# Performance work log

Hardware: AMD Instinct MI355X
Metric: run time of the kernel (lower is better)

## Reference

```python
import jax, jax.numpy as jnp
import numpy as np

N_BOOK = 16  # == len_code; C() loop is only consistent when len_code == n_book


def setup_inputs() -> dict:
    key = jax.random.key(0)
    k1, k2 = jax.random.split(key)
    N = 32768
    D = 256        # len_code * n_book = 16 * 16
    n_classes = 4096
    features = jax.random.normal(k1, (N, D), dtype=jnp.float32)
    # Prototypes passed transposed relative to storage: [len_code*n_book, n_classes]
    Prototypes = jax.random.normal(k2, (D, n_classes), dtype=jnp.float32)
    return {"features": features, "Prototypes": Prototypes}


def reference(features, Prototypes):
    # Faithful to GPQSoftMaxNet.C: per-book matmul, concat over books, mean.
    # features: [N, len_code*n_book] split along dim 1 into chunks of width n_book
    # Prototypes: [len_code*n_book, n_classes] split along dim 0 into chunks of height n_book
    n_book = N_BOOK
    N, D = features.shape
    n_classes = Prototypes.shape[1]
    f = features.reshape(N, -1, n_book)          # [N, n_book(=len_code), n_book]
    P = Prototypes.reshape(-1, n_book, n_classes)  # [n_book(=len_code), n_book, n_classes]
    # mean over books of per-book GEMMs, fused into one einsum (no [N,C,n_book] intermediate)
    logits = jnp.einsum('nbd,bdc->nc', f, P) / jnp.float32(n_book)
    return logits
```

## Files before the change

### kernel.cpp

```cpp
#include <hip/hip_runtime.h>
#include <hip/hip_bf16.h>

typedef __attribute__((ext_vector_type(8))) short short8;
typedef __attribute__((ext_vector_type(4))) float f32x4;

static constexpr int MT = 32768;
static constexpr int KT = 256;
static constexpr int CT = 4096;

__device__ __forceinline__ unsigned short f2b(float f) {
  unsigned int b = __float_as_uint(f);
  b += 0x7FFFu + ((b >> 16) & 1u);
  return (unsigned short)(b >> 16);
}

__global__ void __launch_bounds__(256) cvt_kernel(const float* __restrict__ A,
                                                  const float* __restrict__ B,
                                                  unsigned short* __restrict__ Abf,
                                                  unsigned short* __restrict__ Bt) {
  __shared__ unsigned short tile[32][33];
  int bid = blockIdx.x, tid = threadIdx.x;
  if (bid < 4096) {
    int i = bid * 256 + tid;
    const float4 v0 = reinterpret_cast<const float4*>(A)[2 * i];
    const float4 v1 = reinterpret_cast<const float4*>(A)[2 * i + 1];
    short8 o;
    o[0] = (short)f2b(v0.x); o[1] = (short)f2b(v0.y);
    o[2] = (short)f2b(v0.z); o[3] = (short)f2b(v0.w);
    o[4] = (short)f2b(v1.x); o[5] = (short)f2b(v1.y);
    o[6] = (short)f2b(v1.z); o[7] = (short)f2b(v1.w);
    reinterpret_cast<short8*>(Abf)[i] = o;
  } else {
    int b = bid - 4096;
    int c0 = (b & 127) * 32, k0 = (b >> 7) * 32;
    int tx = tid & 31, ty0 = tid >> 5;
#pragma unroll
    for (int i = 0; i < 4; ++i) {
      int ty = ty0 + i * 8;
      tile[ty][tx] = f2b(B[(size_t)(k0 + ty) * CT + c0 + tx]);
    }
    __syncthreads();
#pragma unroll
    for (int i = 0; i < 4; ++i) {
      int cy = ty0 + i * 8;
      Bt[(size_t)(c0 + cy) * KT + k0 + tx] = tile[tx][cy];
    }
  }
}

__device__ __forceinline__ void gload16(const void* g, void* l) {
  __builtin_amdgcn_global_load_lds(
      (const __attribute__((address_space(1))) void*)g,
      (__attribute__((address_space(3))) void*)l, 16, 0, 0);
}

__global__ void __launch_bounds__(256, 2) gemm_kernel(const unsigned short* __restrict__ Abf,
                                                      const unsigned short* __restrict__ Btw,
                                                      float* __restrict__ O) {
  constexpr int BK = 64;
  __shared__ __align__(16) char smem[48 * 1024];
  unsigned short* Al = (unsigned short*)smem;
  unsigned short* Bl = (unsigned short*)(smem + 16384);
  float* eb = (float*)smem;

  int bid = blockIdx.x;
  int wg = (bid & 7) * 512 + (bid >> 3);
  int tc = wg & 15;
  int tr = wg >> 4;
  int r0 = tr * 128, c0 = tc * 256;

  int tid = threadIdx.x;
  int lane = tid & 63, wid = tid >> 6;
  int wr = wid >> 1, wc = wid & 1;
  int l15 = lane & 15, l4 = lane >> 4;

  f32x4 acc[8][4] = {};

  for (int t = 0; t < KT / BK; ++t) {
    if (t) __syncthreads();
#pragma unroll
    for (int i = 0; i < 4; ++i) {
      int c = i * 256 + wid * 64 + lane;
      int sc = (c & 7) ^ ((c >> 3) & 7);
      gload16(Abf + (size_t)(r0 + (c >> 3)) * KT + t * BK + sc * 8,
              Al + (i * 256 + wid * 64) * 8);
    }
#pragma unroll
    for (int i = 0; i < 8; ++i) {
      int c = i * 256 + wid * 64 + lane;
      int sc = (c & 7) ^ ((c >> 3) & 7);
      gload16(Btw + (size_t)(c0 + (c >> 3)) * KT + t * BK + sc * 8,
              Bl + (i * 256 + wid * 64) * 8);
    }
    __syncthreads();

#pragma unroll
    for (int ks = 0; ks < 2; ++ks) {
      short8 af[4], bf[8];
#pragma unroll
      for (int m = 0; m < 4; ++m) {
        int row = wr * 64 + m * 16 + l15;
        int slot = (ks * 4 + l4) ^ (l15 & 7);
        af[m] = *reinterpret_cast<const short8*>(Al + row * BK + slot * 8);
      }
#pragma unroll
      for (int n = 0; n < 8; ++n) {
        int row = wc * 128 + n * 16 + l15;
        int slot = (ks * 4 + l4) ^ (l15 & 7);
        bf[n] = *reinterpret_cast<const short8*>(Bl + row * BK + slot * 8);
      }
#pragma unroll
      for (int n = 0; n < 8; ++n)
#pragma unroll
        for (int m = 0; m < 4; ++m)
          acc[n][m] = __builtin_amdgcn_mfma_f32_16x16x32_bf16(bf[n], af[m], acc[n][m], 0, 0, 0);
    }
  }

  const float s = 1.0f / 16.0f;
#pragma unroll
  for (int p = 0; p < 4; ++p) {
    __syncthreads();
    if (wr == (p >> 1)) {
#pragma unroll
      for (int mm = 0; mm < 2; ++mm) {
        int m = (p & 1) * 2 + mm;
#pragma unroll
        for (int n = 0; n < 8; ++n) {
          f32x4 v = acc[n][m];
          v[0] *= s; v[1] *= s; v[2] *= s; v[3] *= s;
          *reinterpret_cast<f32x4*>(
              &eb[(mm * 16 + l15) * 264 + wc * 128 + n * 16 + l4 * 4]) = v;
        }
      }
    }
    __syncthreads();
#pragma unroll
    for (int i = 0; i < 8; ++i) {
      int r = i * 4 + wid;
      f32x4 v = *reinterpret_cast<const f32x4*>(&eb[r * 264 + lane * 4]);
      __builtin_nontemporal_store(v, reinterpret_cast<f32x4*>(
          O + (size_t)(r0 + p * 32 + r) * CT + c0 + lane * 4));
    }
  }
}

__global__ void __launch_bounds__(256) naive_kernel(const float* __restrict__ A,
                                                    const float* __restrict__ B,
                                                    float* __restrict__ O) {
  size_t i = (size_t)blockIdx.x * 256 + threadIdx.x;
  int col = (int)(i & (size_t)(CT - 1));
  int row = (int)(i >> 12);
  float s = 0.f;
  for (int k = 0; k < KT; ++k)
    s += A[(size_t)row * KT + k] * B[(size_t)k * CT + col];
  O[i] = s * (1.0f / 16.0f);
}

extern "C" void kernel_launch(void* const* d_in, const int* in_sizes, int n_in,
                              void* d_out, int out_size, void* d_ws, size_t ws_size,
                              hipStream_t stream) {
  const float* A = (const float*)d_in[0];
  const float* B = (const float*)d_in[1];
  float* O = (float*)d_out;
  const size_t needA = (size_t)MT * KT * sizeof(unsigned short);
  const size_t needB = (size_t)CT * KT * sizeof(unsigned short);
  if (ws_size >= needA + needB) {
    unsigned short* Abf = (unsigned short*)d_ws;
    unsigned short* Btw = (unsigned short*)((char*)d_ws + needA);
    cvt_kernel<<<4096 + 1024, 256, 0, stream>>>(A, B, Abf, Btw);
    gemm_kernel<<<(MT / 128) * (CT / 256), 256, 0, stream>>>(Abf, Btw, O);
  } else {
    naive_kernel<<<(unsigned)((size_t)MT * CT / 256), 256, 0, stream>>>(A, B, O);
  }
}
```

Before: 125.9 us.

## Fuse A fp32-to-bf16 conversion into GEMM tile loads

Removes the separate pass that converts features to bf16 in a workspace. The GEMM now loads fp32 A tiles straight into LDS, using a 16-slot XOR swizzle, and rounds them to bf16 in registers before each MFMA. This saves a full read and write of the converted A buffer. In exchange, A traffic into LDS doubles, each A tile is converted redundantly by all 16 column-tile workgroups, and LDS grows to 64KB, which may limit occupancy to 2 blocks.

```diff
diff --git a/kernel.cpp b/kernel.cpp
--- a/kernel.cpp
+++ b/kernel.cpp
@@ -14,37 +14,22 @@
   return (unsigned short)(b >> 16);
 }
 
-__global__ void __launch_bounds__(256) cvt_kernel(const float* __restrict__ A,
-                                                  const float* __restrict__ B,
-                                                  unsigned short* __restrict__ Abf,
-                                                  unsigned short* __restrict__ Bt) {
+__global__ void __launch_bounds__(256) cvtB_kernel(const float* __restrict__ B,
+                                                   unsigned short* __restrict__ Bt) {
   __shared__ unsigned short tile[32][33];
-  int bid = blockIdx.x, tid = threadIdx.x;
-  if (bid < 4096) {
-    int i = bid * 256 + tid;
-    const float4 v0 = reinterpret_cast<const float4*>(A)[2 * i];
-    const float4 v1 = reinterpret_cast<const float4*>(A)[2 * i + 1];
-    short8 o;
-    o[0] = (short)f2b(v0.x); o[1] = (short)f2b(v0.y);
-    o[2] = (short)f2b(v0.z); o[3] = (short)f2b(v0.w);
-    o[4] = (short)f2b(v1.x); o[5] = (short)f2b(v1.y);
-    o[6] = (short)f2b(v1.z); o[7] = (short)f2b(v1.w);
-    reinterpret_cast<short8*>(Abf)[i] = o;
-  } else {
-    int b = bid - 4096;
-    int c0 = (b & 127) * 32, k0 = (b >> 7) * 32;
-    int tx = tid & 31, ty0 = tid >> 5;
+  int b = blockIdx.x, tid = threadIdx.x;
+  int c0 = (b & 127) * 32, k0 = (b >> 7) * 32;
+  int tx = tid & 31, ty0 = tid >> 5;
 #pragma unroll
-    for (int i = 0; i < 4; ++i) {
-      int ty = ty0 + i * 8;
-      tile[ty][tx] = f2b(B[(size_t)(k0 + ty) * CT + c0 + tx]);
-    }
-    __syncthreads();
+  for (int i = 0; i < 4; ++i) {
+    int ty = ty0 + i * 8;
+    tile[ty][tx] = f2b(B[(size_t)(k0 + ty) * CT + c0 + tx]);
+  }
+  __syncthreads();
 #pragma unroll
-    for (int i = 0; i < 4; ++i) {
-      int cy = ty0 + i * 8;
-      Bt[(size_t)(c0 + cy) * KT + k0 + tx] = tile[tx][cy];
-    }
+  for (int i = 0; i < 4; ++i) {
+    int cy = ty0 + i * 8;
+    Bt[(size_t)(c0 + cy) * KT + k0 + tx] = tile[tx][cy];
   }
 }
 
@@ -54,13 +39,13 @@
       (__attribute__((address_space(3))) void*)l, 16, 0, 0);
 }
 
-__global__ void __launch_bounds__(256, 2) gemm_kernel(const unsigned short* __restrict__ Abf,
+__global__ void __launch_bounds__(256, 2) gemm_kernel(const float* __restrict__ A,
                                                       const unsigned short* __restrict__ Btw,
                                                       float* __restrict__ O) {
   constexpr int BK = 64;
-  __shared__ __align__(16) char smem[48 * 1024];
-  unsigned short* Al = (unsigned short*)smem;
-  unsigned short* Bl = (unsigned short*)(smem + 16384);
+  __shared__ __align__(16) char smem[64 * 1024];
+  float* Alf = (float*)smem;
+  unsigned short* Bl = (unsigned short*)(smem + 32768);
   float* eb = (float*)smem;
 
   int bid = blockIdx.x;
@@ -79,11 +64,11 @@
   for (int t = 0; t < KT / BK; ++t) {
     if (t) __syncthreads();
 #pragma unroll
-    for (int i = 0; i < 4; ++i) {
+    for (int i = 0; i < 8; ++i) {
       int c = i * 256 + wid * 64 + lane;
-      int sc = (c & 7) ^ ((c >> 3) & 7);
-      gload16(Abf + (size_t)(r0 + (c >> 3)) * KT + t * BK + sc * 8,
-              Al + (i * 256 + wid * 64) * 8);
+      int sc = (c & 15) ^ ((c >> 4) & 15);
+      gload16(A + (size_t)(r0 + (c >> 4)) * KT + t * BK + sc * 4,
+              Alf + (i * 256 + wid * 64) * 4);
     }
 #pragma unroll
     for (int i = 0; i < 8; ++i) {
@@ -100,8 +85,14 @@
 #pragma unroll
       for (int m = 0; m < 4; ++m) {
         int row = wr * 64 + m * 16 + l15;
-        int slot = (ks * 4 + l4) ^ (l15 & 7);
-        af[m] = *reinterpret_cast<const short8*>(Al + row * BK + slot * 8);
+        int fc = ks * 8 + l4 * 2;
+        f32x4 lo = *reinterpret_cast<const f32x4*>(Alf + row * BK + ((fc ^ l15) * 4));
+        f32x4 hi = *reinterpret_cast<const f32x4*>(Alf + row * BK + (((fc + 1) ^ l15) * 4));
+#pragma unroll
+        for (int j = 0; j < 4; ++j) {
+          af[m][j] = (short)f2b(lo[j]);
+          af[m][4 + j] = (short)f2b(hi[j]);
+        }
       }
 #pragma unroll
       for (int n = 0; n < 8; ++n) {
@@ -163,13 +154,11 @@
   const float* A = (const float*)d_in[0];
   const float* B = (const float*)d_in[1];
   float* O = (float*)d_out;
-  const size_t needA = (size_t)MT * KT * sizeof(unsigned short);
   const size_t needB = (size_t)CT * KT * sizeof(unsigned short);
-  if (ws_size >= needA + needB) {
-    unsigned short* Abf = (unsigned short*)d_ws;
-    unsigned short* Btw = (unsigned short*)((char*)d_ws + needA);
-    cvt_kernel<<<4096 + 1024, 256, 0, stream>>>(A, B, Abf, Btw);
-    gemm_kernel<<<(MT / 128) * (CT / 256), 256, 0, stream>>>(Abf, Btw, O);
+  if (ws_size >= needB) {
+    unsigned short* Btw = (unsigned short*)d_ws;
+    cvtB_kernel<<<1024, 256, 0, stream>>>(B, Btw);
+    gemm_kernel<<<(MT / 128) * (CT / 256), 256, 0, stream>>>(A, Btw, O);
   } else {
     naive_kernel<<<(unsigned)((size_t)MT * CT / 256), 256, 0, stream>>>(A, B, O);
   }
```

Result: slower. 136.4 us (+8.4%).
